# Kernel tuning notes

Measured on AMD Instinct MI355X. Metric: run time of the kernel, lower is better.

Reference implementation:

```python
import jax, jax.numpy as jnp
import numpy as np

N_NODES = 50000
N_EDGES = 800000
F_IN = 128
F_OUT = 128


def setup_inputs() -> dict:
    key = jax.random.key(0)
    k1, k2, k3, k4 = jax.random.split(key, 4)
    x = jax.random.normal(k1, (N_NODES, F_IN), dtype=jnp.float32)
    edge_index = jax.random.randint(k2, (2, N_EDGES), 0, N_NODES, dtype=jnp.int64)
    edge_weight = jax.random.uniform(k3, (N_EDGES,), dtype=jnp.float32)
    # GCNConv linear weight (applied as x @ W) and bias
    W = jax.random.normal(k4, (F_IN, F_OUT), dtype=jnp.float32) / np.sqrt(F_IN)
    b = jnp.zeros((F_OUT,), dtype=jnp.float32)
    return {"x": x, "edge_index": edge_index, "edge_weight": edge_weight, "W": W, "b": b}


def reference(x, edge_index, edge_weight, W, b):
    """Single GCNConv forward (PyG semantics: normalize=True, add_self_loops=True).

    out[i] = sum_{(j->i) in E'} norm_ji * (x[j] @ W) + b
    where E' = E + self loops (weight 1), norm = D^{-1/2} A D^{-1/2}.
    """
    n = x.shape[0]
    # add self loops with weight 1.0
    loops = jnp.arange(n, dtype=edge_index.dtype)
    row = jnp.concatenate([edge_index[0], loops])  # source nodes
    col = jnp.concatenate([edge_index[1], loops])  # target nodes
    ew = jnp.concatenate([edge_weight, jnp.ones((n,), dtype=edge_weight.dtype)])
    # symmetric degree normalization (degree computed at targets, as in PyG gcn_norm)
    deg = jax.ops.segment_sum(ew, col, num_segments=n)
    dinv = jnp.where(deg > 0, jax.lax.rsqrt(deg), 0.0)
    norm = dinv[row] * ew * dinv[col]  # [E+N]
    # linear transform then gather-scale-scatter aggregation
    h = x @ W  # [N, F_OUT]
    msgs = norm[:, None] * h[row]  # [E+N, F_OUT]
    out = jax.ops.segment_sum(msgs, col, num_segments=n) + b
    return out
```

## Files before the change

kernel.cpp:

```cpp
#include <hip/hip_runtime.h>


#define F 128
#define MAXOVF 4096
#define SHIFT 8
#define RNG 256
#define NBMAX 256
#define SA_BS 1024
#define SA_EPB 4096

typedef __attribute__((ext_vector_type(8))) short bf16x8;
typedef __attribute__((ext_vector_type(4))) float f32x4;

__device__ __forceinline__ unsigned bf16rne(float f) {
    unsigned u = __float_as_uint(f);
    return (u + 0x7fffu + ((u >> 16) & 1u)) >> 16;
}
__device__ __forceinline__ float bflo(unsigned u) { return __uint_as_float(u << 16); }
__device__ __forceinline__ float bfhi(unsigned u) { return __uint_as_float(u & 0xffff0000u); }

__global__ __launch_bounds__(1024) void sortA_k(
        const int* __restrict__ row, const int* __restrict__ col,
        const float* __restrict__ ew, const float* __restrict__ x,
        const float* __restrict__ W,
        unsigned* __restrict__ gcnt,
        unsigned long long* __restrict__ stage,
        unsigned* __restrict__ ovf_w, int* __restrict__ ovf, int* __restrict__ ovfc,
        uint4* __restrict__ xb4, unsigned short* __restrict__ Wt,
        int E, int NB, int capb, int SAB, int XB4, long ng8) {
    int tid = threadIdx.x;
    int blk = blockIdx.x;
    if (blk >= SAB) {
        if (blk < SAB + XB4) {
            long i = (long)(blk - SAB) * 1024 + tid;
            if (i < ng8) {
                const float4* x4 = (const float4*)x;
                float4 a = x4[2 * i], c = x4[2 * i + 1];
                uint4 o;
                o.x = bf16rne(a.x) | (bf16rne(a.y) << 16);
                o.y = bf16rne(a.z) | (bf16rne(a.w) << 16);
                o.z = bf16rne(c.x) | (bf16rne(c.y) << 16);
                o.w = bf16rne(c.z) | (bf16rne(c.w) << 16);
                xb4[i] = o;
            }
        } else {
            int idx = (blk - SAB - XB4) * 1024 + tid;
            if (idx < F * F) {
                int k = idx >> 7, nn = idx & 127;
                Wt[nn * F + k] = (unsigned short)bf16rne(W[idx]);
            }
        }
        return;
    }
    __shared__ unsigned hist[NBMAX], sc[NBMAX], rbase[NBMAX], ravail[NBMAX];
    __shared__ unsigned long long stg[SA_EPB];
    unsigned xcc;
    asm volatile("s_getreg_b32 %0, hwreg(HW_REG_XCC_ID, 0, 4)" : "=s"(xcc));
    xcc &= 7u;
    long e0 = (long)blk * SA_EPB;
    for (int i = tid; i < NBMAX; i += SA_BS) hist[i] = 0;
    __syncthreads();
    unsigned long long pk[4];
    int bk[4]; unsigned rk[4];
    #pragma unroll
    for (int k = 0; k < 4; ++k) {
        long e = e0 + k * SA_BS + tid;
        bk[k] = -1;
        if (e < E) {
            int c = col[e], r = row[e];
            float w = ew[e];
            unsigned wq = __float2uint_rn(w * 32768.0f);
            if (wq > 32767u) wq = 32767u;
            pk[k] = ((unsigned long long)(unsigned)c << 32) |
                    ((unsigned long long)(unsigned)r << 15) | wq;
            bk[k] = c >> SHIFT;
            rk[k] = atomicAdd(&hist[bk[k]], 1u);
        }
    }
    __syncthreads();
    if (tid < NBMAX) sc[tid] = hist[tid];
    __syncthreads();
    for (int d = 1; d < NBMAX; d <<= 1) {
        unsigned v = 0;
        if (tid < NBMAX && tid >= d) v = sc[tid - d];
        __syncthreads();
        if (tid < NBMAX) sc[tid] += v;
        __syncthreads();
    }
    if (tid < NB) {
        unsigned cnt = hist[tid], bs = 0, av = 0;
        if (cnt > 0) {
            bs = atomicAdd(&gcnt[xcc * NBMAX + tid], cnt);
            av = (bs < (unsigned)capb) ? ((unsigned)capb - bs) : 0u;
        }
        rbase[tid] = bs;
        ravail[tid] = av;
    }
    __syncthreads();
    #pragma unroll
    for (int k = 0; k < 4; ++k)
        if (bk[k] >= 0) stg[sc[bk[k]] - hist[bk[k]] + rk[k]] = pk[k];
    __syncthreads();
    int tot = (int)sc[NBMAX - 1];
    for (int i = tid; i < tot; i += SA_BS) {
        int lo = 0, hi = NB - 1;
        while (lo < hi) {
            int mid = (lo + hi + 1) >> 1;
            if (sc[mid] - hist[mid] <= (unsigned)i) lo = mid; else hi = mid - 1;
        }
        unsigned j = (unsigned)i - (sc[lo] - hist[lo]);
        unsigned long long v = stg[i];
        if (j < ravail[lo]) {
            stage[((size_t)lo * 8 + xcc) * capb + rbase[lo] + j] = v;
        } else {
            int c = (int)(v >> 32);
            int r = (int)((v >> 15) & 0x1FFFFu);
            unsigned wq = (unsigned)(v & 0x7FFFu);
            atomicAdd(&ovf_w[c], wq);
            int p = atomicAdd(ovfc, 1);
            if (p < MAXOVF) {
                ovf[3 * p] = r; ovf[3 * p + 1] = c; ovf[3 * p + 2] = (int)wq;
            }
        }
    }
}

__global__ __launch_bounds__(1024) void sortB_k(
        const unsigned long long* __restrict__ stage,
        const unsigned* __restrict__ gcnt, const unsigned* __restrict__ ovf_w,
        unsigned* __restrict__ eout, int* __restrict__ offA, int* __restrict__ cntA,
        float* __restrict__ dinv, int n, int capb) {
    __shared__ unsigned cnt[RNG], wsum[RNG], scn[RNG], bex[RNG];
    int tid = threadIdx.x;
    int b = blockIdx.x;
    int node0 = b << SHIFT;
    int nodes = n - node0; if (nodes > RNG) nodes = RNG; if (nodes < 0) nodes = 0;
    for (int i = tid; i < RNG; i += 1024) { cnt[i] = 0; wsum[i] = 0; }
    __syncthreads();
    for (int xr = 0; xr < 8; ++xr) {
        unsigned m = gcnt[xr * NBMAX + b]; if (m > (unsigned)capb) m = capb;
        const unsigned long long* rg = stage + ((size_t)b * 8 + xr) * capb;
        for (unsigned i = tid; i < m; i += 1024) {
            unsigned long long v = rg[i];
            int no = (int)(v >> 32) - node0;
            atomicAdd(&cnt[no], 1u);
            atomicAdd(&wsum[no], (unsigned)(v & 0x7FFFu));
        }
    }
    __syncthreads();
    if (tid < RNG) scn[tid] = cnt[tid];
    __syncthreads();
    for (int d = 1; d < RNG; d <<= 1) {
        unsigned v = 0;
        if (tid < RNG && tid >= d) v = scn[tid - d];
        __syncthreads();
        if (tid < RNG) scn[tid] += v;
        __syncthreads();
    }
    if (tid < RNG) bex[tid] = scn[tid] - cnt[tid];
    __syncthreads();
    if (tid < nodes) {
        int node = node0 + tid;
        float deg = (float)(wsum[tid] + ovf_w[node]) * (1.0f / 32768.0f) + 1.0f;
        dinv[node] = rsqrtf(deg);
        offA[node] = b * (capb * 8) + (int)bex[tid];
        cntA[node] = (int)cnt[tid];
    }
    __syncthreads();
    for (int i = tid; i < RNG; i += 1024) cnt[i] = 0;
    __syncthreads();
    for (int xr = 0; xr < 8; ++xr) {
        unsigned m = gcnt[xr * NBMAX + b]; if (m > (unsigned)capb) m = capb;
        const unsigned long long* rg = stage + ((size_t)b * 8 + xr) * capb;
        for (unsigned i = tid; i < m; i += 1024) {
            unsigned long long v = rg[i];
            int no = (int)(v >> 32) - node0;
            unsigned rkk = atomicAdd(&cnt[no], 1u);
            unsigned pos = (unsigned)(b * (capb * 8)) + bex[no] + rkk;
            eout[pos] = (unsigned)((((v >> 15) & 0x1FFFFu) << 15) | (v & 0x7FFFu));
        }
    }
}

__global__ __launch_bounds__(256) void aggregate_k(
        const uint4* __restrict__ xb4, const float* __restrict__ dinv,
        const int* __restrict__ offA, const int* __restrict__ cntA,
        const unsigned* __restrict__ eout, uint4* __restrict__ yb4, int n) {
    int lane = threadIdx.x & 63, wv = threadIdx.x >> 6;
    int g = lane >> 4, l = lane & 15;
    int i = blockIdx.x * 16 + wv * 4 + g;
    if (i >= n) return;
    float di = dinv[i];
    uint4 xs = xb4[(size_t)i * 16 + l];
    float a0 = di * bflo(xs.x), a1 = di * bfhi(xs.x);
    float a2 = di * bflo(xs.y), a3 = di * bfhi(xs.y);
    float a4 = di * bflo(xs.z), a5 = di * bfhi(xs.z);
    float a6 = di * bflo(xs.w), a7 = di * bfhi(xs.w);
    int cnt = cntA[i], off = offA[i];
    for (int bb = 0; bb < cnt; bb += 32) {
        int e0 = bb + 2 * l;
        unsigned m0 = (e0     < cnt) ? eout[off + e0]     : 0u;
        unsigned m1 = (e0 + 1 < cnt) ? eout[off + e0 + 1] : 0u;
        int sv0 = (int)(m0 >> 15), sv1 = (int)(m1 >> 15);
        float wk0 = (float)(m0 & 0x7FFFu) * (1.0f / 32768.0f) * dinv[sv0];
        float wk1 = (float)(m1 & 0x7FFFu) * (1.0f / 32768.0f) * dinv[sv1];
        int cb = cnt - bb; if (cb > 32) cb = 32;
        for (int j0 = 0; j0 < cb; j0 += 8) {
            int base = g * 16 + (j0 >> 1);
            int   s0 = __shfl(sv0, base),     s1 = __shfl(sv1, base);
            int   s2 = __shfl(sv0, base + 1), s3 = __shfl(sv1, base + 1);
            int   s4 = __shfl(sv0, base + 2), s5 = __shfl(sv1, base + 2);
            int   s6 = __shfl(sv0, base + 3), s7 = __shfl(sv1, base + 3);
            float w0 = __shfl(wk0, base),     w1 = __shfl(wk1, base);
            float w2 = __shfl(wk0, base + 1), w3 = __shfl(wk1, base + 1);
            float w4 = __shfl(wk0, base + 2), w5 = __shfl(wk1, base + 2);
            float w6 = __shfl(wk0, base + 3), w7 = __shfl(wk1, base + 3);
            uint4 u0 = xb4[(size_t)s0 * 16 + l];
            uint4 u1 = xb4[(size_t)s1 * 16 + l];
            uint4 u2 = xb4[(size_t)s2 * 16 + l];
            uint4 u3 = xb4[(size_t)s3 * 16 + l];
            uint4 u4 = xb4[(size_t)s4 * 16 + l];
            uint4 u5 = xb4[(size_t)s5 * 16 + l];
            uint4 u6 = xb4[(size_t)s6 * 16 + l];
            uint4 u7 = xb4[(size_t)s7 * 16 + l];
            a0 += w0 * bflo(u0.x) + w1 * bflo(u1.x) + w2 * bflo(u2.x) + w3 * bflo(u3.x)
                + w4 * bflo(u4.x) + w5 * bflo(u5.x) + w6 * bflo(u6.x) + w7 * bflo(u7.x);
            a1 += w0 * bfhi(u0.x) + w1 * bfhi(u1.x) + w2 * bfhi(u2.x) + w3 * bfhi(u3.x)
                + w4 * bfhi(u4.x) + w5 * bfhi(u5.x) + w6 * bfhi(u6.x) + w7 * bfhi(u7.x);
            a2 += w0 * bflo(u0.y) + w1 * bflo(u1.y) + w2 * bflo(u2.y) + w3 * bflo(u3.y)
                + w4 * bflo(u4.y) + w5 * bflo(u5.y) + w6 * bflo(u6.y) + w7 * bflo(u7.y);
            a3 += w0 * bfhi(u0.y) + w1 * bfhi(u1.y) + w2 * bfhi(u2.y) + w3 * bfhi(u3.y)
                + w4 * bfhi(u4.y) + w5 * bfhi(u5.y) + w6 * bfhi(u6.y) + w7 * bfhi(u7.y);
            a4 += w0 * bflo(u0.z) + w1 * bflo(u1.z) + w2 * bflo(u2.z) + w3 * bflo(u3.z)
                + w4 * bflo(u4.z) + w5 * bflo(u5.z) + w6 * bflo(u6.z) + w7 * bflo(u7.z);
            a5 += w0 * bfhi(u0.z) + w1 * bfhi(u1.z) + w2 * bfhi(u2.z) + w3 * bfhi(u3.z)
                + w4 * bfhi(u4.z) + w5 * bfhi(u5.z) + w6 * bfhi(u6.z) + w7 * bfhi(u7.z);
            a6 += w0 * bflo(u0.w) + w1 * bflo(u1.w) + w2 * bflo(u2.w) + w3 * bflo(u3.w)
                + w4 * bflo(u4.w) + w5 * bflo(u5.w) + w6 * bflo(u6.w) + w7 * bflo(u7.w);
            a7 += w0 * bfhi(u0.w) + w1 * bfhi(u1.w) + w2 * bfhi(u2.w) + w3 * bfhi(u3.w)
                + w4 * bfhi(u4.w) + w5 * bfhi(u5.w) + w6 * bfhi(u6.w) + w7 * bfhi(u7.w);
        }
    }
    a0 *= di; a1 *= di; a2 *= di; a3 *= di;
    a4 *= di; a5 *= di; a6 *= di; a7 *= di;
    uint4 o;
    o.x = bf16rne(a0) | (bf16rne(a1) << 16);
    o.y = bf16rne(a2) | (bf16rne(a3) << 16);
    o.z = bf16rne(a4) | (bf16rne(a5) << 16);
    o.w = bf16rne(a6) | (bf16rne(a7) << 16);
    yb4[(size_t)i * 16 + l] = o;
}

__global__ void fix_k(const unsigned* __restrict__ xb, const float* __restrict__ dinv,
                      const int* __restrict__ ovf, const int* __restrict__ ovfc,
                      unsigned* __restrict__ yb) {
    int cnt = *ovfc;
    if (cnt > MAXOVF) cnt = MAXOVF;
    int l = threadIdx.x;
    for (int k = 0; k < cnt; ++k) {
        int src = ovf[3 * k], c = ovf[3 * k + 1];
        float w = (float)ovf[3 * k + 2] * (1.0f / 32768.0f);
        float wk = w * dinv[src] * dinv[c];
        unsigned u = xb[(size_t)src * 64 + l];
        unsigned y = yb[(size_t)c * 64 + l];
        float y0 = bflo(y) + wk * bflo(u);
        float y1 = bfhi(y) + wk * bfhi(u);
        yb[(size_t)c * 64 + l] = bf16rne(y0) | (bf16rne(y1) << 16);
    }
}

__global__ __launch_bounds__(256) void gemm_k(const unsigned short* __restrict__ yb,
        const unsigned short* __restrict__ Wt, const float* __restrict__ bias,
        float* __restrict__ out, int n) {
    int tid = threadIdx.x;
    int w = tid >> 6, lane = tid & 63;
    int m = lane & 15, q = lane >> 4;
    int r0 = blockIdx.x * 64 + w * 16;
    int ar = r0 + m;
    if (ar >= n) ar = n - 1;
    const unsigned short* arow = yb + (size_t)ar * F + q * 8;

    f32x4 acc[8];
    #pragma unroll
    for (int t = 0; t < 8; ++t) acc[t] = (f32x4){0.f, 0.f, 0.f, 0.f};

    #pragma unroll
    for (int kk = 0; kk < 4; ++kk) {
        bf16x8 a = *(const bf16x8*)(arow + kk * 32);
        #pragma unroll
        for (int t = 0; t < 8; ++t) {
            bf16x8 bfr = *(const bf16x8*)(Wt + (size_t)(t * 16 + m) * F + kk * 32 + q * 8);
            acc[t] = __builtin_amdgcn_mfma_f32_16x16x32_bf16(a, bfr, acc[t], 0, 0, 0);
        }
    }

    int orow = r0 + q * 4;
    #pragma unroll
    for (int t = 0; t < 8; ++t) {
        float bv = bias[t * 16 + m];
        #pragma unroll
        for (int v = 0; v < 4; ++v) {
            int rr = orow + v;
            if (rr < n) out[(size_t)rr * F + t * 16 + m] = acc[t][v] + bv;
        }
    }
}

extern "C" void kernel_launch(void* const* d_in, const int* in_sizes, int n_in,
                              void* d_out, int out_size, void* d_ws, size_t ws_size,
                              hipStream_t stream) {
    const float* x  = (const float*)d_in[0];
    const int*   ei = (const int*)d_in[1];
    const float* ew = (const float*)d_in[2];
    const float* W  = (const float*)d_in[3];
    const float* b  = (const float*)d_in[4];
    float* out = (float*)d_out;

    int n = in_sizes[0] / F;
    int E = in_sizes[2];
    const int* row = ei;
    const int* col = ei + E;
    int NB = (n + RNG - 1) >> SHIFT;

    float* ws = (float*)d_ws;
    size_t o = 0;
    auto take = [&](size_t elems) { size_t r = o; o += (elems + 63) & ~63ull; return r; };
    size_t o_gcnt  = take(8 * NBMAX);
    size_t o_ovfc  = take(64);
    size_t o_ovfw  = take(n);
    size_t zero_end = o;
    size_t o_ovf   = take((size_t)MAXOVF * 3);
    size_t o_dinv  = take(n);
    size_t o_offA  = take(n);
    size_t o_cntA  = take(n);
    size_t o_wt    = take(F * F / 2);
    size_t o_xb    = take((size_t)n * (F / 2));
    size_t o_yb    = take((size_t)n * (F / 2));
    size_t units = ws_size / 4;
    size_t remain = (units > o + 128) ? (units - o - 128) : 0;
    int capb = (int)(remain / ((size_t)NB * 8 * 3));
    if (capb > 2048) capb = 2048;
    if (capb < 256)  capb = 256;
    size_t o_stage = take((size_t)NB * 8 * capb * 2);
    size_t o_eout  = take((size_t)NB * 8 * capb);
    (void)n_in; (void)out_size; (void)o_eout;

    unsigned* gcnt = (unsigned*)(ws + o_gcnt);
    int*      ovfc = (int*)(ws + o_ovfc);
    unsigned* ovfw = (unsigned*)(ws + o_ovfw);
    int*      ovf  = (int*)(ws + o_ovf);
    float*    dinv = ws + o_dinv;
    int*      offA = (int*)(ws + o_offA);
    int*      cntA = (int*)(ws + o_cntA);
    unsigned short* Wt = (unsigned short*)(ws + o_wt);
    unsigned* xb   = (unsigned*)(ws + o_xb);
    unsigned* yb   = (unsigned*)(ws + o_yb);
    unsigned long long* stage = (unsigned long long*)(ws + o_stage);
    unsigned* eout = (unsigned*)(ws + o_eout);

    hipMemsetAsync(d_ws, 0, zero_end * sizeof(float), stream);

    int SAB = (E + SA_EPB - 1) / SA_EPB;
    long ng8 = (long)n * (F / 8);
    int XB4 = (int)((ng8 + 1023) / 1024);
    int WB = (F * F + 1023) / 1024;

    sortA_k<<<SAB + XB4 + WB, SA_BS, 0, stream>>>(row, col, ew, x, W, gcnt, stage,
                                                  ovfw, ovf, ovfc, (uint4*)xb, Wt,
                                                  E, NB, capb, SAB, XB4, ng8);
    sortB_k<<<NB, SA_BS, 0, stream>>>(stage, gcnt, ovfw, eout, offA, cntA,
                                      dinv, n, capb);
    aggregate_k<<<(n + 15) / 16, 256, 0, stream>>>((const uint4*)xb, dinv, offA,
                                                   cntA, eout, (uint4*)yb, n);
    fix_k<<<1, 64, 0, stream>>>(xb, dinv, ovf, ovfc, yb);
    gemm_k<<<(n + 63) / 64, 256, 0, stream>>>((const unsigned short*)yb, Wt, b, out, n);
}
```

Baseline: 156.8 us.

## Single-pass sortB with register-held entries, fuse overflow fix, coalesced GEMM stores

Halves the bucket range to 128 nodes so there are twice as many sortB blocks, and rewrites sortB to read the stage buffer once, keeping each entry and its rank in registers instead of re-reading everything in a second pass. The separate single-block fix_k kernel is removed and overflow edges are handled inside aggregate_k, which saves a launch but makes every thread read ovfc and scan the overflow list when it is nonempty. The GEMM epilogue stages results through shared memory so output is written as coalesced float4 rows. The per-thread register arrays assume at most 8 entries per thread, which the capb cap of 1024 guarantees.

```diff
diff --git a/kernel.cpp b/kernel.cpp
--- a/kernel.cpp
+++ b/kernel.cpp
@@ -3,9 +3,9 @@
 
 #define F 128
 #define MAXOVF 4096
-#define SHIFT 8
-#define RNG 256
-#define NBMAX 256
+#define SHIFT 7
+#define RNG 128
+#define NBMAX 512
 #define SA_BS 1024
 #define SA_EPB 4096
 
@@ -131,21 +131,36 @@
         unsigned* __restrict__ eout, int* __restrict__ offA, int* __restrict__ cntA,
         float* __restrict__ dinv, int n, int capb) {
     __shared__ unsigned cnt[RNG], wsum[RNG], scn[RNG], bex[RNG];
+    __shared__ unsigned rpre[9];
     int tid = threadIdx.x;
     int b = blockIdx.x;
     int node0 = b << SHIFT;
     int nodes = n - node0; if (nodes > RNG) nodes = RNG; if (nodes < 0) nodes = 0;
-    for (int i = tid; i < RNG; i += 1024) { cnt[i] = 0; wsum[i] = 0; }
-    __syncthreads();
-    for (int xr = 0; xr < 8; ++xr) {
-        unsigned m = gcnt[xr * NBMAX + b]; if (m > (unsigned)capb) m = capb;
-        const unsigned long long* rg = stage + ((size_t)b * 8 + xr) * capb;
-        for (unsigned i = tid; i < m; i += 1024) {
-            unsigned long long v = rg[i];
-            int no = (int)(v >> 32) - node0;
-            atomicAdd(&cnt[no], 1u);
-            atomicAdd(&wsum[no], (unsigned)(v & 0x7FFFu));
-        }
+    if (tid < RNG) { cnt[tid] = 0; wsum[tid] = 0; }
+    if (tid == 0) {
+        unsigned acc = 0; rpre[0] = 0;
+        #pragma unroll
+        for (int xr = 0; xr < 8; ++xr) {
+            unsigned m = gcnt[xr * NBMAX + b]; if (m > (unsigned)capb) m = capb;
+            acc += m; rpre[xr + 1] = acc;
+        }
+    }
+    __syncthreads();
+    int T = (int)rpre[8];
+    unsigned ent[8]; unsigned short noa[8], rka[8];
+    int myc = 0;
+    for (int i = tid; i < T; i += 1024) {
+        int xr = 0;
+        while (rpre[xr + 1] <= (unsigned)i) ++xr;
+        unsigned j = (unsigned)i - rpre[xr];
+        unsigned long long v = stage[((size_t)b * 8 + xr) * capb + j];
+        int no = (int)(v >> 32) - node0;
+        unsigned wq = (unsigned)(v & 0x7FFFu);
+        unsigned rk = atomicAdd(&cnt[no], 1u);
+        atomicAdd(&wsum[no], wq);
+        ent[myc] = (unsigned)((((v >> 15) & 0x1FFFFu) << 15) | wq);
+        noa[myc] = (unsigned short)no; rka[myc] = (unsigned short)rk;
+        ++myc;
     }
     __syncthreads();
     if (tid < RNG) scn[tid] = cnt[tid];
@@ -166,26 +181,17 @@
         offA[node] = b * (capb * 8) + (int)bex[tid];
         cntA[node] = (int)cnt[tid];
     }
-    __syncthreads();
-    for (int i = tid; i < RNG; i += 1024) cnt[i] = 0;
-    __syncthreads();
-    for (int xr = 0; xr < 8; ++xr) {
-        unsigned m = gcnt[xr * NBMAX + b]; if (m > (unsigned)capb) m = capb;
-        const unsigned long long* rg = stage + ((size_t)b * 8 + xr) * capb;
-        for (unsigned i = tid; i < m; i += 1024) {
-            unsigned long long v = rg[i];
-            int no = (int)(v >> 32) - node0;
-            unsigned rkk = atomicAdd(&cnt[no], 1u);
-            unsigned pos = (unsigned)(b * (capb * 8)) + bex[no] + rkk;
-            eout[pos] = (unsigned)((((v >> 15) & 0x1FFFFu) << 15) | (v & 0x7FFFu));
-        }
-    }
+    unsigned base = (unsigned)(b * (capb * 8));
+    for (int k = 0; k < myc; ++k)
+        eout[base + bex[noa[k]] + rka[k]] = ent[k];
 }
 
 __global__ __launch_bounds__(256) void aggregate_k(
         const uint4* __restrict__ xb4, const float* __restrict__ dinv,
         const int* __restrict__ offA, const int* __restrict__ cntA,
-        const unsigned* __restrict__ eout, uint4* __restrict__ yb4, int n) {
+        const unsigned* __restrict__ eout,
+        const int* __restrict__ ovf, const int* __restrict__ ovfc,
+        uint4* __restrict__ yb4, int n) {
     int lane = threadIdx.x & 63, wv = threadIdx.x >> 6;
     int g = lane >> 4, l = lane & 15;
     int i = blockIdx.x * 16 + wv * 4 + g;
@@ -241,6 +247,21 @@
                 + w4 * bfhi(u4.w) + w5 * bfhi(u5.w) + w6 * bfhi(u6.w) + w7 * bfhi(u7.w);
         }
     }
+    int oc = *ovfc;
+    if (oc > 0) {
+        if (oc > MAXOVF) oc = MAXOVF;
+        for (int k = 0; k < oc; ++k) {
+            if (ovf[3 * k + 1] == i) {
+                int sv = ovf[3 * k];
+                float wk = (float)ovf[3 * k + 2] * (1.0f / 32768.0f) * dinv[sv];
+                uint4 u = xb4[(size_t)sv * 16 + l];
+                a0 += wk * bflo(u.x); a1 += wk * bfhi(u.x);
+                a2 += wk * bflo(u.y); a3 += wk * bfhi(u.y);
+                a4 += wk * bflo(u.z); a5 += wk * bfhi(u.z);
+                a6 += wk * bflo(u.w); a7 += wk * bfhi(u.w);
+            }
+        }
+    }
     a0 *= di; a1 *= di; a2 *= di; a3 *= di;
     a4 *= di; a5 *= di; a6 *= di; a7 *= di;
     uint4 o;
@@ -251,27 +272,10 @@
     yb4[(size_t)i * 16 + l] = o;
 }
 
-__global__ void fix_k(const unsigned* __restrict__ xb, const float* __restrict__ dinv,
-                      const int* __restrict__ ovf, const int* __restrict__ ovfc,
-                      unsigned* __restrict__ yb) {
-    int cnt = *ovfc;
-    if (cnt > MAXOVF) cnt = MAXOVF;
-    int l = threadIdx.x;
-    for (int k = 0; k < cnt; ++k) {
-        int src = ovf[3 * k], c = ovf[3 * k + 1];
-        float w = (float)ovf[3 * k + 2] * (1.0f / 32768.0f);
-        float wk = w * dinv[src] * dinv[c];
-        unsigned u = xb[(size_t)src * 64 + l];
-        unsigned y = yb[(size_t)c * 64 + l];
-        float y0 = bflo(y) + wk * bflo(u);
-        float y1 = bfhi(y) + wk * bfhi(u);
-        yb[(size_t)c * 64 + l] = bf16rne(y0) | (bf16rne(y1) << 16);
-    }
-}
-
 __global__ __launch_bounds__(256) void gemm_k(const unsigned short* __restrict__ yb,
         const unsigned short* __restrict__ Wt, const float* __restrict__ bias,
         float* __restrict__ out, int n) {
+    __shared__ float cs[4][16 * 132];
     int tid = threadIdx.x;
     int w = tid >> 6, lane = tid & 63;
     int m = lane & 15, q = lane >> 4;
@@ -294,15 +298,21 @@
         }
     }
 
-    int orow = r0 + q * 4;
-    #pragma unroll
-    for (int t = 0; t < 8; ++t) {
-        float bv = bias[t * 16 + m];
+    float* csw = cs[w];
+    #pragma unroll
+    for (int t = 0; t < 8; ++t)
         #pragma unroll
-        for (int v = 0; v < 4; ++v) {
-            int rr = orow + v;
-            if (rr < n) out[(size_t)rr * F + t * 16 + m] = acc[t][v] + bv;
-        }
+        for (int v = 0; v < 4; ++v)
+            csw[(q * 4 + v) * 132 + t * 16 + m] = acc[t][v];
+    int cg = lane & 31;
+    float4 bv4 = ((const float4*)bias)[cg];
+    #pragma unroll
+    for (int rp = 0; rp < 8; ++rp) {
+        int rowl = rp * 2 + (lane >> 5);
+        int rr = r0 + rowl;
+        float4 v4 = *(float4*)&csw[rowl * 132 + cg * 4];
+        v4.x += bv4.x; v4.y += bv4.y; v4.z += bv4.z; v4.w += bv4.w;
+        if (rr < n) ((float4*)out)[(size_t)rr * 32 + cg] = v4;
     }
 }
 
@@ -339,7 +349,7 @@
     size_t units = ws_size / 4;
     size_t remain = (units > o + 128) ? (units - o - 128) : 0;
     int capb = (int)(remain / ((size_t)NB * 8 * 3));
-    if (capb > 2048) capb = 2048;
+    if (capb > 1024) capb = 1024;
     if (capb < 256)  capb = 256;
     size_t o_stage = take((size_t)NB * 8 * capb * 2);
     size_t o_eout  = take((size_t)NB * 8 * capb);
@@ -371,7 +381,7 @@
     sortB_k<<<NB, SA_BS, 0, stream>>>(stage, gcnt, ovfw, eout, offA, cntA,
                                       dinv, n, capb);
     aggregate_k<<<(n + 15) / 16, 256, 0, stream>>>((const uint4*)xb, dinv, offA,
-                                                   cntA, eout, (uint4*)yb, n);
-    fix_k<<<1, 64, 0, stream>>>(xb, dinv, ovf, ovfc, yb);
+                                                   cntA, eout, ovf, ovfc,
+                                                   (uint4*)yb, n);
     gemm_k<<<(n + 63) / 64, 256, 0, stream>>>((const unsigned short*)yb, Wt, b, out, n);
 }
```

After: 150.9 us. 1.04x faster.
